# Kernel tuning notes

Measured on AMD Instinct MI355X. Metric: run time of the kernel, lower is better.

The kernel has to match this reference:

```python
import jax, jax.numpy as jnp
import numpy as np

D_MODEL = 768
EXPAND = 2
D_INNER = EXPAND * D_MODEL  # 1536
D_STATE = 16
D_CONV = 4
DT_RANK = D_MODEL // 16  # 48
N_LAYER = 3
BATCH, SEQLEN = 2, 1024
EPS = 1e-5


def setup_inputs() -> dict:
    key = jax.random.key(0)
    ks = jax.random.split(key, 8)
    s = 0.02
    hidden_states = jax.random.normal(ks[0], (BATCH, SEQLEN, D_MODEL), jnp.float32)
    norm_w = jnp.ones((N_LAYER, D_MODEL), jnp.float32)
    in_proj_w = s * jax.random.normal(ks[1], (N_LAYER, 2 * D_INNER, D_MODEL), jnp.float32)
    conv_w = s * jax.random.normal(ks[2], (N_LAYER, D_INNER, D_CONV), jnp.float32)
    conv_b = jnp.zeros((N_LAYER, D_INNER), jnp.float32)
    x_proj_w = s * jax.random.normal(ks[3], (N_LAYER, DT_RANK + 2 * D_STATE, D_INNER), jnp.float32)
    dt_proj_w = s * jax.random.normal(ks[4], (N_LAYER, D_INNER, DT_RANK), jnp.float32)
    dt_proj_b = jnp.full((N_LAYER, D_INNER), -4.6, jnp.float32)  # softplus ~ 0.01
    # S4D-real init: A_log = log(1..d_state), tiled over channels
    A_log = jnp.tile(jnp.log(jnp.arange(1, D_STATE + 1, dtype=jnp.float32))[None, None, :], (N_LAYER, D_INNER, 1))
    D_skip = jnp.ones((N_LAYER, D_INNER), jnp.float32)
    out_proj_w = s * jax.random.normal(ks[5], (N_LAYER, D_MODEL, D_INNER), jnp.float32)
    norm_f_w = jnp.ones((D_MODEL,), jnp.float32)
    return dict(hidden_states=hidden_states, norm_w=norm_w, in_proj_w=in_proj_w,
                conv_w=conv_w, conv_b=conv_b, x_proj_w=x_proj_w, dt_proj_w=dt_proj_w,
                dt_proj_b=dt_proj_b, A_log=A_log, D_skip=D_skip, out_proj_w=out_proj_w,
                norm_f_w=norm_f_w)


def _rmsnorm(x, w):
    return x * jax.lax.rsqrt(jnp.mean(x * x, axis=-1, keepdims=True) + EPS) * w


def _causal_conv1d(x, w, b):
    # x: [B, L, D]; w: [D, K] depthwise; left-pad for causality
    xt = jnp.transpose(x, (0, 2, 1))  # [B, D, L]
    y = jax.lax.conv_general_dilated(xt, w[:, None, :], window_strides=(1,),
                                     padding=[(D_CONV - 1, 0)], feature_group_count=D_INNER)
    return jnp.transpose(y, (0, 2, 1)) + b


def _selective_scan(u, delta, A, Bc, Cc, Dp):
    # u, delta: [B, L, D]; A: [D, N]; Bc, Cc: [B, L, N]
    def step(h, inp):
        dt, bt, ct, ut = inp  # [B,D], [B,N], [B,N], [B,D]
        h = jnp.exp(dt[..., None] * A) * h + (dt * ut)[..., None] * bt[:, None, :]
        y = jnp.einsum('bdn,bn->bd', h, ct)
        return h, y
    h0 = jnp.zeros((u.shape[0], u.shape[2], A.shape[1]), u.dtype)
    xs = (jnp.swapaxes(delta, 0, 1), jnp.swapaxes(Bc, 0, 1), jnp.swapaxes(Cc, 0, 1), jnp.swapaxes(u, 0, 1))
    _, ys = jax.lax.scan(step, h0, xs)  # ys: [L, B, D]
    return jnp.swapaxes(ys, 0, 1) + u * Dp


def _mixer(h, in_w, cw, cb, xw, dtw, dtb, A_log, Dp, ow):
    xz = jnp.einsum('bld,ed->ble', h, in_w)  # [B, L, 2*D_INNER]
    x, z = xz[..., :D_INNER], xz[..., D_INNER:]
    x = jax.nn.silu(_causal_conv1d(x, cw, cb))
    x_dbl = jnp.einsum('bld,ed->ble', x, xw)
    dt = x_dbl[..., :DT_RANK]
    Bc = x_dbl[..., DT_RANK:DT_RANK + D_STATE]
    Cc = x_dbl[..., DT_RANK + D_STATE:]
    delta = jax.nn.softplus(jnp.einsum('blr,dr->bld', dt, dtw) + dtb)
    A = -jnp.exp(A_log)
    y = _selective_scan(x, delta, A, Bc, Cc, Dp)
    y = y * jax.nn.silu(z)
    return jnp.einsum('bld,ed->ble', y, ow)


def reference(hidden_states, norm_w, in_proj_w, conv_w, conv_b, x_proj_w, dt_proj_w,
              dt_proj_b, A_log, D_skip, out_proj_w, norm_f_w):
    hidden = hidden_states
    residual = None
    for i in range(N_LAYER):
        residual = hidden if residual is None else hidden + residual  # fused add
        hidden = _rmsnorm(residual, norm_w[i])
        hidden = _mixer(hidden, in_proj_w[i], conv_w[i], conv_b[i], x_proj_w[i],
                        dt_proj_w[i], dt_proj_b[i], A_log[i], D_skip[i], out_proj_w[i])
    # final fused add + RMSNorm (prenorm=False)
    return _rmsnorm(hidden + residual, norm_f_w)
```

## Files before the change

### kernel.cpp

```cpp
#include <hip/hip_runtime.h>
#include <math.h>

#define D_MODEL 768
#define D_INNER 1536
#define D_STATE 16
#define D_CONV 4
#define DT_RANK 48
#define N_LAYER 3
#define BATCH 2
#define SEQLEN 1024
#define NROWS (BATCH * SEQLEN)
#define XDBL_W (DT_RANK + 2 * D_STATE)
#define EPS 1e-5f

#define SCLEN 16
#define SDN 16
#define KSPLIT_X 8

typedef short bf16x8 __attribute__((ext_vector_type(8)));
typedef float f32x4 __attribute__((ext_vector_type(4)));

__device__ __forceinline__ ushort f2bf(float x) {
    union { float f; uint u; } v; v.f = x;
    uint r = v.u + 0x7fff + ((v.u >> 16) & 1);
    return (ushort)(r >> 16);
}

__device__ __forceinline__ void gload_lds16(const void* g, void* l) {
    __builtin_amdgcn_global_load_lds(
        (const __attribute__((address_space(1))) unsigned int*)g,
        (__attribute__((address_space(3))) unsigned int*)l, 16, 0, 0);
}

__global__ __launch_bounds__(256) void cvt_bf16_kernel(
    const float* __restrict__ s, ushort* __restrict__ d, int n4)
{
    int i = blockIdx.x * 256 + threadIdx.x;
    if (i >= n4) return;
    float4 v = ((const float4*)s)[i];
    ushort4 o;
    o.x = f2bf(v.x); o.y = f2bf(v.y); o.z = f2bf(v.z); o.w = f2bf(v.w);
    ((ushort4*)d)[i] = o;
}

__global__ __launch_bounds__(256) void cvt_xw_pad_kernel(
    const float* __restrict__ src, ushort* __restrict__ dst)
{
    const int per = 128 * 1536 / 4;
    int i = blockIdx.x * 256 + threadIdx.x;
    if (i >= 3 * per) return;
    int li = i / per, rem = i - li * per;
    int r = (rem * 4) / 1536, c = (rem * 4) % 1536;
    ushort4 o = make_ushort4(0, 0, 0, 0);
    if (r < XDBL_W) {
        const float* s = src + ((size_t)li * XDBL_W + r) * 1536 + c;
        o.x = f2bf(s[0]); o.y = f2bf(s[1]); o.z = f2bf(s[2]); o.w = f2bf(s[3]);
    }
    ((ushort4*)dst)[i] = o;
}

__global__ __launch_bounds__(256) void cvt_dtw_pad_kernel(
    const float* __restrict__ src, ushort* __restrict__ dst)
{
    const int per = 1536 * 64 / 4;
    int i = blockIdx.x * 256 + threadIdx.x;
    if (i >= 3 * per) return;
    int li = i / per, rem = i - li * per;
    int r = (rem * 4) / 64, c = (rem * 4) % 64;
    ushort4 o = make_ushort4(0, 0, 0, 0);
    if (c < DT_RANK) {
        const float* s = src + ((size_t)li * 1536 + r) * DT_RANK + c;
        o.x = f2bf(s[0]); o.y = f2bf(s[1]); o.z = f2bf(s[2]); o.w = f2bf(s[3]);
    }
    ((ushort4*)dst)[i] = o;
}

__global__ __launch_bounds__(256) void add_rmsnorm_kernel(
    const float* __restrict__ x, const float* __restrict__ res_in,
    const float* __restrict__ w, float* __restrict__ res_out,
    float* __restrict__ normed_f32, ushort* __restrict__ normed_bf)
{
    int row = blockIdx.x;
    int tid = threadIdx.x;
    const float* xr = x + row * D_MODEL;
    float v[3];
    float ss = 0.f;
#pragma unroll
    for (int i = 0; i < 3; i++) {
        int c = tid + i * 256;
        float t = xr[c];
        if (res_in) t += res_in[row * D_MODEL + c];
        v[i] = t;
        ss += t * t;
    }
    for (int off = 32; off; off >>= 1) ss += __shfl_xor(ss, off, 64);
    __shared__ float red[4];
    if ((tid & 63) == 0) red[tid >> 6] = ss;
    __syncthreads();
    float tot = red[0] + red[1] + red[2] + red[3];
    float scale = rsqrtf(tot * (1.f / D_MODEL) + EPS);
#pragma unroll
    for (int i = 0; i < 3; i++) {
        int c = tid + i * 256;
        if (res_out) res_out[row * D_MODEL + c] = v[i];
        float o = v[i] * scale * w[c];
        if (normed_f32) normed_f32[row * D_MODEL + c] = o;
        if (normed_bf)  normed_bf[row * D_MODEL + c] = f2bf(o);
    }
}

template <int BM, int BN, int EPI, int SPLITK>
__global__ __launch_bounds__(256) void gemm_mfma_kernel(
    const ushort* __restrict__ A, const ushort* __restrict__ W,
    const float* __restrict__ bias, float* __restrict__ C,
    int ldc, int Nout, int M, int K)
{
    constexpr int TM = BM / 32;
    constexpr int TN = BN / 32;
    __shared__ __attribute__((aligned(16))) ushort As[BM * 64];
    __shared__ __attribute__((aligned(16))) ushort Ws[BN * 64];
    const int t = threadIdx.x;
    const int lane = t & 63, w = t >> 6;
    const int ln15 = lane & 15, q = lane >> 4;
    const int row0 = blockIdx.y * BM, col0 = blockIdx.x * BN;
    const int wm0 = (w & 1) * (BM / 2), wn0 = (w >> 1) * (BN / 2);

    int kper = K / SPLITK;
    int kz = (SPLITK > 1) ? blockIdx.z * kper : 0;
    if (SPLITK > 1) C += (size_t)blockIdx.z * M * ldc;

    f32x4 acc[TM][TN];
#pragma unroll
    for (int i = 0; i < TM; i++)
#pragma unroll
        for (int j = 0; j < TN; j++) acc[i][j] = (f32x4){0.f, 0.f, 0.f, 0.f};

    for (int k0 = kz; k0 < kz + kper; k0 += 64) {
        __syncthreads();
#pragma unroll
        for (int i = 0; i < BM / 32; i++) {
            int p = (i * 4 + w) * 64 + lane;
            int r = p >> 3, s = p & 7;
            int g = s ^ (r & 7);
            gload_lds16(A + (size_t)(row0 + r) * K + k0 + g * 8, &As[p * 8]);
        }
#pragma unroll
        for (int i = 0; i < BN / 32; i++) {
            int p = (i * 4 + w) * 64 + lane;
            int r = p >> 3, s = p & 7;
            int g = s ^ (r & 7);
            gload_lds16(W + (size_t)(col0 + r) * K + k0 + g * 8, &Ws[p * 8]);
        }
        __syncthreads();
#pragma unroll
        for (int ks = 0; ks < 2; ks++) {
            bf16x8 af[TM], wf[TN];
#pragma unroll
            for (int im = 0; im < TM; im++) {
                int m = wm0 + im * 16 + ln15;
                int slot = (ks * 4 + q) ^ (m & 7);
                af[im] = *(const bf16x8*)&As[m * 64 + slot * 8];
            }
#pragma unroll
            for (int jn = 0; jn < TN; jn++) {
                int n = wn0 + jn * 16 + ln15;
                int slot = (ks * 4 + q) ^ (n & 7);
                wf[jn] = *(const bf16x8*)&Ws[n * 64 + slot * 8];
            }
#pragma unroll
            for (int im = 0; im < TM; im++)
#pragma unroll
                for (int jn = 0; jn < TN; jn++)
                    acc[im][jn] = __builtin_amdgcn_mfma_f32_16x16x32_bf16(
                        af[im], wf[jn], acc[im][jn], 0, 0, 0);
        }
    }
#pragma unroll
    for (int im = 0; im < TM; im++) {
#pragma unroll
        for (int jn = 0; jn < TN; jn++) {
            int rr = row0 + wm0 + im * 16 + q * 4;
            int cc = col0 + wn0 + jn * 16 + ln15;
            if (cc < Nout) {
                float* cp = C + (size_t)rr * ldc + cc;
#pragma unroll
                for (int r = 0; r < 4; r++) {
                    float v = acc[im][jn][r];
                    if (EPI == 1) {
                        v += bias[cc];
                        v = (v > 20.f) ? v : log1pf(__expf(v));
                    }
                    cp[(size_t)r * ldc] = v;
                }
            }
        }
    }
}

__global__ __launch_bounds__(256) void xreduce_kernel(
    const float* __restrict__ Cp, float* __restrict__ xdbl,
    ushort* __restrict__ xdt)
{
    const int S4 = NROWS * XDBL_W / 4;
    int i = blockIdx.x * 256 + threadIdx.x;
    if (i >= S4) return;
    const float4* p = (const float4*)Cp;
    float4 o = p[i];
#pragma unroll
    for (int z = 1; z < KSPLIT_X; z++) {
        float4 a = p[i + (size_t)z * S4];
        o.x += a.x; o.y += a.y; o.z += a.z; o.w += a.w;
    }
    ((float4*)xdbl)[i] = o;
    int row = (i * 4) / XDBL_W, c0 = (i * 4) % XDBL_W;
    if (c0 < DT_RANK) {
        ushort4 b;
        b.x = f2bf(o.x); b.y = f2bf(o.y); b.z = f2bf(o.z); b.w = f2bf(o.w);
        *(ushort4*)&xdt[(size_t)row * 64 + c0] = b;
    } else if (c0 < 64) {
        *(ushort4*)&xdt[(size_t)row * 64 + c0] = make_ushort4(0, 0, 0, 0);
    }
}

__global__ __launch_bounds__(256) void conv_silu_kernel(
    const float* __restrict__ xz, const float* __restrict__ cw,
    const float* __restrict__ cb, float* __restrict__ out,
    ushort* __restrict__ out_bf)
{
    int idx = blockIdx.x * 256 + threadIdx.x;
    int d = idx % D_INNER;
    int bl = idx / D_INNER;
    int l = bl % SEQLEN;
    float s = cb[d];
    const float* xp = xz + (size_t)bl * (2 * D_INNER) + d;
#pragma unroll
    for (int k = 0; k < D_CONV; k++) {
        int ls = l - (D_CONV - 1) + k;
        if (ls >= 0) s += cw[d * D_CONV + k] * xp[(k - (D_CONV - 1)) * (2 * D_INNER)];
    }
    float sil = s / (1.f + __expf(-s));
    out[(size_t)bl * D_INNER + d] = sil;
    out_bf[(size_t)bl * D_INNER + d] = f2bf(sil);
}

__global__ __launch_bounds__(1024) void scan2_kernel(
    const float* __restrict__ u, const float* __restrict__ delta,
    const float* __restrict__ A_log, const float* __restrict__ xdbl,
    const float* __restrict__ Dskip, const float* __restrict__ xz,
    ushort* __restrict__ ybf)
{
    __shared__ float PL[16][SDN * 17];
    __shared__ float HL[16][SDN * 17];
    const int t = threadIdx.x;
    const int lane = t & 63;
    const int w = t >> 6;
    const int dsub = lane & 15;
    const int csub = lane >> 4;
    const int c = w * 4 + csub;
    const int b = blockIdx.x / (D_INNER / SDN);
    const int d = (blockIdx.x % (D_INNER / SDN)) * SDN + dsub;

    float a2[D_STATE];
#pragma unroll
    for (int n = 0; n < D_STATE; n++)
        a2[n] = -__expf(A_log[d * D_STATE + n]) * 1.44269504f;

    const size_t base = (size_t)b * SEQLEN * D_INNER + d;
    const float* dtp = delta + base;
    const float* up  = u + base;
    const float* xrow = xdbl + (size_t)b * SEQLEN * XDBL_W;
    const int l0 = c * SCLEN;

    float h[D_STATE], P[D_STATE];
#pragma unroll
    for (int n = 0; n < D_STATE; n++) { h[n] = 0.f; P[n] = 1.f; }

    for (int i = 0; i < SCLEN; i++) {
        const int l = l0 + i;
        float dt = dtp[(size_t)l * D_INNER];
        float uu = up[(size_t)l * D_INNER];
        const float4* Bv = (const float4*)(xrow + (size_t)l * XDBL_W + DT_RANK);
        float4 q0 = Bv[0], q1 = Bv[1], q2 = Bv[2], q3 = Bv[3];
        float Bf[D_STATE] = {q0.x,q0.y,q0.z,q0.w, q1.x,q1.y,q1.z,q1.w,
                             q2.x,q2.y,q2.z,q2.w, q3.x,q3.y,q3.z,q3.w};
        float dtu = dt * uu;
#pragma unroll
        for (int n = 0; n < D_STATE; n++) {
            float e = __builtin_amdgcn_exp2f(dt * a2[n]);
            P[n] *= e;
            h[n] = e * h[n] + dtu * Bf[n];
        }
    }

#pragma unroll
    for (int n = 0; n < D_STATE; n++) {
        float Pp = __shfl(P[n], lane - 16, 64);
        float Hp = __shfl(h[n], lane - 16, 64);
        bool act = csub >= 1;
        h[n] = act ? P[n] * Hp + h[n] : h[n];
        P[n] = act ? P[n] * Pp : P[n];
    }
#pragma unroll
    for (int n = 0; n < D_STATE; n++) {
        float Pp = __shfl(P[n], lane - 32, 64);
        float Hp = __shfl(h[n], lane - 32, 64);
        bool act = csub >= 2;
        h[n] = act ? P[n] * Hp + h[n] : h[n];
        P[n] = act ? P[n] * Pp : P[n];
    }

    if (csub == 3) {
#pragma unroll
        for (int n = 0; n < D_STATE; n++) {
            PL[w][dsub * 17 + n] = P[n];
            HL[w][dsub * 17 + n] = h[n];
        }
    }
    __syncthreads();

    if (t < SDN * D_STATE) {
        const int d2 = t >> 4, n2 = t & 15;
        float hin = 0.f;
        for (int ww = 0; ww < 16; ww++) {
            float Pw = PL[ww][d2 * 17 + n2];
            float Hw = HL[ww][d2 * 17 + n2];
            HL[ww][d2 * 17 + n2] = hin;
            hin = Pw * hin + Hw;
        }
    }
    __syncthreads();

#pragma unroll
    for (int n = 0; n < D_STATE; n++) {
        float Win = HL[w][dsub * 17 + n];
        float Pe = __shfl(P[n], lane - 16, 64);
        float He = __shfl(h[n], lane - 16, 64);
        h[n] = (csub == 0) ? Win : Pe * Win + He;
    }

    const float Dsk = Dskip[d];
    const float* zp = xz + (size_t)b * SEQLEN * (2 * D_INNER) + D_INNER + d;
    ushort* yp = ybf + base;
    for (int i = 0; i < SCLEN; i++) {
        const int l = l0 + i;
        float dt = dtp[(size_t)l * D_INNER];
        float uu = up[(size_t)l * D_INNER];
        float zz = zp[(size_t)l * (2 * D_INNER)];
        const float4* Bv = (const float4*)(xrow + (size_t)l * XDBL_W + DT_RANK);
        float4 q0 = Bv[0], q1 = Bv[1], q2 = Bv[2], q3 = Bv[3];
        float4 r0 = Bv[4], r1 = Bv[5], r2 = Bv[6], r3 = Bv[7];
        float Bf[D_STATE] = {q0.x,q0.y,q0.z,q0.w, q1.x,q1.y,q1.z,q1.w,
                             q2.x,q2.y,q2.z,q2.w, q3.x,q3.y,q3.z,q3.w};
        float Cf[D_STATE] = {r0.x,r0.y,r0.z,r0.w, r1.x,r1.y,r1.z,r1.w,
                             r2.x,r2.y,r2.z,r2.w, r3.x,r3.y,r3.z,r3.w};
        float dtu = dt * uu;
        float acc = 0.f;
#pragma unroll
        for (int n = 0; n < D_STATE; n++) {
            float e = __builtin_amdgcn_exp2f(dt * a2[n]);
            h[n] = e * h[n] + dtu * Bf[n];
            acc += h[n] * Cf[n];
        }
        float yy = acc + uu * Dsk;
        float ee = __builtin_amdgcn_exp2f(-zz * 1.44269504f);
        float sil = zz * __builtin_amdgcn_rcpf(1.f + ee);
        yp[(size_t)l * D_INNER] = f2bf(yy * sil);
    }
}

extern "C" void kernel_launch(void* const* d_in, const int* in_sizes, int n_in,
                              void* d_out, int out_size, void* d_ws, size_t ws_size,
                              hipStream_t stream)
{
    const float* hs        = (const float*)d_in[0];
    const float* norm_w    = (const float*)d_in[1];
    const float* in_proj_w = (const float*)d_in[2];
    const float* conv_w    = (const float*)d_in[3];
    const float* conv_b    = (const float*)d_in[4];
    const float* x_proj_w  = (const float*)d_in[5];
    const float* dt_proj_w = (const float*)d_in[6];
    const float* dt_proj_b = (const float*)d_in[7];
    const float* A_log     = (const float*)d_in[8];
    const float* D_skip    = (const float*)d_in[9];
    const float* out_proj_w= (const float*)d_in[10];
    const float* norm_f_w  = (const float*)d_in[11];

    float* ws = (float*)d_ws;
    float* residual = ws;
    float* hidden   = residual + NROWS * D_MODEL;
    float* xz       = hidden + NROWS * D_MODEL;
    float* xconv    = xz + NROWS * 2 * D_INNER;
    float* xdbl     = xconv + NROWS * D_INNER;
    float* delta    = xdbl + NROWS * XDBL_W;
    float* xpart    = delta + NROWS * D_INNER;
    ushort* normbf  = (ushort*)(xpart + (size_t)KSPLIT_X * NROWS * XDBL_W);
    ushort* ybf     = normbf + NROWS * D_MODEL;
    ushort* xconvbf = ybf + NROWS * D_INNER;
    ushort* xdtbf   = xconvbf + NROWS * D_INNER;
    ushort* win_bf  = xdtbf + NROWS * 64;
    ushort* wout_bf = win_bf + (size_t)N_LAYER * 2 * D_INNER * D_MODEL;
    ushort* xw_pad  = wout_bf + (size_t)N_LAYER * D_MODEL * D_INNER;
    ushort* dtw_pad = xw_pad + (size_t)N_LAYER * 128 * 1536;

    {
        int n_in4  = N_LAYER * 2 * D_INNER * D_MODEL / 4;
        int n_out4 = N_LAYER * D_MODEL * D_INNER / 4;
        cvt_bf16_kernel<<<(n_in4 + 255) / 256, 256, 0, stream>>>(in_proj_w, win_bf, n_in4);
        cvt_bf16_kernel<<<(n_out4 + 255) / 256, 256, 0, stream>>>(out_proj_w, wout_bf, n_out4);
        cvt_xw_pad_kernel<<<(3 * 128 * 1536 / 4 + 255) / 256, 256, 0, stream>>>(x_proj_w, xw_pad);
        cvt_dtw_pad_kernel<<<(3 * 1536 * 64 / 4 + 255) / 256, 256, 0, stream>>>(dt_proj_w, dtw_pad);
    }

    for (int i = 0; i < N_LAYER; i++) {
        add_rmsnorm_kernel<<<NROWS, 256, 0, stream>>>(
            i == 0 ? hs : hidden, i == 0 ? nullptr : residual,
            norm_w + i * D_MODEL, residual, nullptr, normbf);
        gemm_mfma_kernel<64, 128, 0, 1><<<dim3(2 * D_INNER / 128, NROWS / 64), 256, 0, stream>>>(
            normbf, win_bf + (size_t)i * 2 * D_INNER * D_MODEL, nullptr,
            xz, 2 * D_INNER, 2 * D_INNER, NROWS, D_MODEL);
        conv_silu_kernel<<<NROWS * D_INNER / 256, 256, 0, stream>>>(
            xz, conv_w + i * D_INNER * D_CONV, conv_b + i * D_INNER, xconv, xconvbf);
        gemm_mfma_kernel<64, 128, 0, KSPLIT_X><<<dim3(1, NROWS / 64, KSPLIT_X), 256, 0, stream>>>(
            xconvbf, xw_pad + (size_t)i * 128 * 1536, nullptr,
            xpart, XDBL_W, XDBL_W, NROWS, D_INNER);
        xreduce_kernel<<<(NROWS * XDBL_W / 4 + 255) / 256, 256, 0, stream>>>(
            xpart, xdbl, xdtbf);
        gemm_mfma_kernel<128, 128, 1, 1><<<dim3(D_INNER / 128, NROWS / 128), 256, 0, stream>>>(
            xdtbf, dtw_pad + (size_t)i * 1536 * 64, dt_proj_b + i * D_INNER,
            delta, D_INNER, D_INNER, NROWS, 64);
        scan2_kernel<<<BATCH * (D_INNER / SDN), 1024, 0, stream>>>(
            xconv, delta, A_log + (size_t)i * D_INNER * D_STATE, xdbl,
            D_skip + i * D_INNER, xz, ybf);
        gemm_mfma_kernel<64, 64, 0, 1><<<dim3(D_MODEL / 64, NROWS / 64), 256, 0, stream>>>(
            ybf, wout_bf + (size_t)i * D_MODEL * D_INNER, nullptr,
            hidden, D_MODEL, D_MODEL, NROWS, D_INNER);
    }
    add_rmsnorm_kernel<<<NROWS, 256, 0, stream>>>(
        hidden, residual, norm_f_w, nullptr, (float*)d_out, nullptr);
}
```

Before: 497.9 us.

## Store xz and conv output in bf16, drop split-K x_proj, merge weight converts

The in_proj GEMM now writes xz directly as bf16, and the conv kernel emits only bf16, so the scan reads u and z as bf16. The split-K x_proj GEMM and its reduction kernel are replaced by a single 32-row-tile GEMM whose epilogue writes the fp32 xdbl and the padded bf16 dt input. The four weight-conversion kernels merge into one launch, and the dt_proj tile size changes. These steps cut intermediate memory traffic and launch count, at the cost of bf16 rounding on u and z inside the scan and less parallelism in the x_proj GEMM.

```diff
diff --git a/kernel.cpp b/kernel.cpp
--- a/kernel.cpp
+++ b/kernel.cpp
@@ -15,7 +15,6 @@
 
 #define SCLEN 16
 #define SDN 16
-#define KSPLIT_X 8
 
 typedef short bf16x8 __attribute__((ext_vector_type(8)));
 typedef float f32x4 __attribute__((ext_vector_type(4)));
@@ -25,6 +24,10 @@
     uint r = v.u + 0x7fff + ((v.u >> 16) & 1);
     return (ushort)(r >> 16);
 }
+__device__ __forceinline__ float bf2f(ushort x) {
+    union { uint u; float f; } v; v.u = ((uint)x) << 16;
+    return v.f;
+}
 
 __device__ __forceinline__ void gload_lds16(const void* g, void* l) {
     __builtin_amdgcn_global_load_lds(
@@ -32,47 +35,54 @@
         (__attribute__((address_space(3))) unsigned int*)l, 16, 0, 0);
 }
 
-__global__ __launch_bounds__(256) void cvt_bf16_kernel(
-    const float* __restrict__ s, ushort* __restrict__ d, int n4)
+#define CVT_N0 (3 * 3072 * 768 / 4)
+#define CVT_N1 (3 * 768 * 1536 / 4)
+#define CVT_N2 (3 * 128 * 1536 / 4)
+#define CVT_N3 (3 * 1536 * 64 / 4)
+#define CVT_C1 (CVT_N0)
+#define CVT_C2 (CVT_C1 + CVT_N1)
+#define CVT_C3 (CVT_C2 + CVT_N2)
+#define CVT_TOT (CVT_C3 + CVT_N3)
+
+__global__ __launch_bounds__(256) void cvt_all_kernel(
+    const float* __restrict__ w_in, const float* __restrict__ w_out,
+    const float* __restrict__ w_x, const float* __restrict__ w_dt,
+    ushort* __restrict__ d_in, ushort* __restrict__ d_out,
+    ushort* __restrict__ d_x, ushort* __restrict__ d_dt)
 {
     int i = blockIdx.x * 256 + threadIdx.x;
-    if (i >= n4) return;
-    float4 v = ((const float4*)s)[i];
-    ushort4 o;
-    o.x = f2bf(v.x); o.y = f2bf(v.y); o.z = f2bf(v.z); o.w = f2bf(v.w);
-    ((ushort4*)d)[i] = o;
-}
-
-__global__ __launch_bounds__(256) void cvt_xw_pad_kernel(
-    const float* __restrict__ src, ushort* __restrict__ dst)
-{
-    const int per = 128 * 1536 / 4;
-    int i = blockIdx.x * 256 + threadIdx.x;
-    if (i >= 3 * per) return;
-    int li = i / per, rem = i - li * per;
-    int r = (rem * 4) / 1536, c = (rem * 4) % 1536;
-    ushort4 o = make_ushort4(0, 0, 0, 0);
-    if (r < XDBL_W) {
-        const float* s = src + ((size_t)li * XDBL_W + r) * 1536 + c;
-        o.x = f2bf(s[0]); o.y = f2bf(s[1]); o.z = f2bf(s[2]); o.w = f2bf(s[3]);
-    }
-    ((ushort4*)dst)[i] = o;
-}
-
-__global__ __launch_bounds__(256) void cvt_dtw_pad_kernel(
-    const float* __restrict__ src, ushort* __restrict__ dst)
-{
-    const int per = 1536 * 64 / 4;
-    int i = blockIdx.x * 256 + threadIdx.x;
-    if (i >= 3 * per) return;
-    int li = i / per, rem = i - li * per;
-    int r = (rem * 4) / 64, c = (rem * 4) % 64;
-    ushort4 o = make_ushort4(0, 0, 0, 0);
-    if (c < DT_RANK) {
-        const float* s = src + ((size_t)li * 1536 + r) * DT_RANK + c;
-        o.x = f2bf(s[0]); o.y = f2bf(s[1]); o.z = f2bf(s[2]); o.w = f2bf(s[3]);
-    }
-    ((ushort4*)dst)[i] = o;
+    if (i < CVT_C1) {
+        float4 v = ((const float4*)w_in)[i];
+        ushort4 o; o.x = f2bf(v.x); o.y = f2bf(v.y); o.z = f2bf(v.z); o.w = f2bf(v.w);
+        ((ushort4*)d_in)[i] = o;
+    } else if (i < CVT_C2) {
+        int j = i - CVT_C1;
+        float4 v = ((const float4*)w_out)[j];
+        ushort4 o; o.x = f2bf(v.x); o.y = f2bf(v.y); o.z = f2bf(v.z); o.w = f2bf(v.w);
+        ((ushort4*)d_out)[j] = o;
+    } else if (i < CVT_C3) {
+        int j = i - CVT_C2;
+        const int per = 128 * 1536 / 4;
+        int li = j / per, rem = j - li * per;
+        int r = (rem * 4) / 1536, c = (rem * 4) % 1536;
+        ushort4 o = make_ushort4(0, 0, 0, 0);
+        if (r < XDBL_W) {
+            const float* s = w_x + ((size_t)li * XDBL_W + r) * 1536 + c;
+            o.x = f2bf(s[0]); o.y = f2bf(s[1]); o.z = f2bf(s[2]); o.w = f2bf(s[3]);
+        }
+        ((ushort4*)d_x)[j] = o;
+    } else if (i < CVT_TOT) {
+        int j = i - CVT_C3;
+        const int per = 1536 * 64 / 4;
+        int li = j / per, rem = j - li * per;
+        int r = (rem * 4) / 64, c = (rem * 4) % 64;
+        ushort4 o = make_ushort4(0, 0, 0, 0);
+        if (c < DT_RANK) {
+            const float* s = w_dt + ((size_t)li * 1536 + r) * DT_RANK + c;
+            o.x = f2bf(s[0]); o.y = f2bf(s[1]); o.z = f2bf(s[2]); o.w = f2bf(s[3]);
+        }
+        ((ushort4*)d_dt)[j] = o;
+    }
 }
 
 __global__ __launch_bounds__(256) void add_rmsnorm_kernel(
@@ -109,11 +119,11 @@
     }
 }
 
-template <int BM, int BN, int EPI, int SPLITK>
+template <int BM, int BN, int EPI, int OUTBF>
 __global__ __launch_bounds__(256) void gemm_mfma_kernel(
     const ushort* __restrict__ A, const ushort* __restrict__ W,
-    const float* __restrict__ bias, float* __restrict__ C,
-    int ldc, int Nout, int M, int K)
+    const float* __restrict__ bias, void* __restrict__ Cv,
+    ushort* __restrict__ C2, int ldc, int Nout, int M, int K)
 {
     constexpr int TM = BM / 32;
     constexpr int TN = BN / 32;
@@ -125,9 +135,8 @@
     const int row0 = blockIdx.y * BM, col0 = blockIdx.x * BN;
     const int wm0 = (w & 1) * (BM / 2), wn0 = (w >> 1) * (BN / 2);
 
-    int kper = K / SPLITK;
-    int kz = (SPLITK > 1) ? blockIdx.z * kper : 0;
-    if (SPLITK > 1) C += (size_t)blockIdx.z * M * ldc;
+    float* Cf = (float*)Cv;
+    ushort* Cb = (ushort*)Cv;
 
     f32x4 acc[TM][TN];
 #pragma unroll
@@ -135,7 +144,7 @@
 #pragma unroll
         for (int j = 0; j < TN; j++) acc[i][j] = (f32x4){0.f, 0.f, 0.f, 0.f};
 
-    for (int k0 = kz; k0 < kz + kper; k0 += 64) {
+    for (int k0 = 0; k0 < K; k0 += 64) {
         __syncthreads();
 #pragma unroll
         for (int i = 0; i < BM / 32; i++) {
@@ -181,72 +190,49 @@
         for (int jn = 0; jn < TN; jn++) {
             int rr = row0 + wm0 + im * 16 + q * 4;
             int cc = col0 + wn0 + jn * 16 + ln15;
-            if (cc < Nout) {
-                float* cp = C + (size_t)rr * ldc + cc;
-#pragma unroll
-                for (int r = 0; r < 4; r++) {
-                    float v = acc[im][jn][r];
+#pragma unroll
+            for (int r = 0; r < 4; r++) {
+                float v = acc[im][jn][r];
+                if (EPI == 2) {
+                    if (cc < Nout) Cf[(size_t)(rr + r) * ldc + cc] = v;
+                    if (cc < DT_RANK)  C2[(size_t)(rr + r) * 64 + cc] = f2bf(v);
+                    else if (cc < 64)  C2[(size_t)(rr + r) * 64 + cc] = 0;
+                } else if (cc < Nout) {
                     if (EPI == 1) {
                         v += bias[cc];
                         v = (v > 20.f) ? v : log1pf(__expf(v));
                     }
-                    cp[(size_t)r * ldc] = v;
+                    if (OUTBF) Cb[(size_t)(rr + r) * ldc + cc] = f2bf(v);
+                    else       Cf[(size_t)(rr + r) * ldc + cc] = v;
                 }
             }
         }
     }
 }
 
-__global__ __launch_bounds__(256) void xreduce_kernel(
-    const float* __restrict__ Cp, float* __restrict__ xdbl,
-    ushort* __restrict__ xdt)
-{
-    const int S4 = NROWS * XDBL_W / 4;
-    int i = blockIdx.x * 256 + threadIdx.x;
-    if (i >= S4) return;
-    const float4* p = (const float4*)Cp;
-    float4 o = p[i];
-#pragma unroll
-    for (int z = 1; z < KSPLIT_X; z++) {
-        float4 a = p[i + (size_t)z * S4];
-        o.x += a.x; o.y += a.y; o.z += a.z; o.w += a.w;
-    }
-    ((float4*)xdbl)[i] = o;
-    int row = (i * 4) / XDBL_W, c0 = (i * 4) % XDBL_W;
-    if (c0 < DT_RANK) {
-        ushort4 b;
-        b.x = f2bf(o.x); b.y = f2bf(o.y); b.z = f2bf(o.z); b.w = f2bf(o.w);
-        *(ushort4*)&xdt[(size_t)row * 64 + c0] = b;
-    } else if (c0 < 64) {
-        *(ushort4*)&xdt[(size_t)row * 64 + c0] = make_ushort4(0, 0, 0, 0);
-    }
-}
-
 __global__ __launch_bounds__(256) void conv_silu_kernel(
-    const float* __restrict__ xz, const float* __restrict__ cw,
-    const float* __restrict__ cb, float* __restrict__ out,
-    ushort* __restrict__ out_bf)
+    const ushort* __restrict__ xzbf, const float* __restrict__ cw,
+    const float* __restrict__ cb, ushort* __restrict__ out_bf)
 {
     int idx = blockIdx.x * 256 + threadIdx.x;
     int d = idx % D_INNER;
     int bl = idx / D_INNER;
     int l = bl % SEQLEN;
     float s = cb[d];
-    const float* xp = xz + (size_t)bl * (2 * D_INNER) + d;
+    const ushort* xp = xzbf + (size_t)bl * (2 * D_INNER) + d;
 #pragma unroll
     for (int k = 0; k < D_CONV; k++) {
         int ls = l - (D_CONV - 1) + k;
-        if (ls >= 0) s += cw[d * D_CONV + k] * xp[(k - (D_CONV - 1)) * (2 * D_INNER)];
+        if (ls >= 0) s += cw[d * D_CONV + k] * bf2f(xp[(k - (D_CONV - 1)) * (2 * D_INNER)]);
     }
     float sil = s / (1.f + __expf(-s));
-    out[(size_t)bl * D_INNER + d] = sil;
     out_bf[(size_t)bl * D_INNER + d] = f2bf(sil);
 }
 
 __global__ __launch_bounds__(1024) void scan2_kernel(
-    const float* __restrict__ u, const float* __restrict__ delta,
+    const ushort* __restrict__ ubf, const float* __restrict__ delta,
     const float* __restrict__ A_log, const float* __restrict__ xdbl,
-    const float* __restrict__ Dskip, const float* __restrict__ xz,
+    const float* __restrict__ Dskip, const ushort* __restrict__ xzbf,
     ushort* __restrict__ ybf)
 {
     __shared__ float PL[16][SDN * 17];
@@ -267,7 +253,7 @@
 
     const size_t base = (size_t)b * SEQLEN * D_INNER + d;
     const float* dtp = delta + base;
-    const float* up  = u + base;
+    const ushort* up = ubf + base;
     const float* xrow = xdbl + (size_t)b * SEQLEN * XDBL_W;
     const int l0 = c * SCLEN;
 
@@ -278,7 +264,7 @@
     for (int i = 0; i < SCLEN; i++) {
         const int l = l0 + i;
         float dt = dtp[(size_t)l * D_INNER];
-        float uu = up[(size_t)l * D_INNER];
+        float uu = bf2f(up[(size_t)l * D_INNER]);
         const float4* Bv = (const float4*)(xrow + (size_t)l * XDBL_W + DT_RANK);
         float4 q0 = Bv[0], q1 = Bv[1], q2 = Bv[2], q3 = Bv[3];
         float Bf[D_STATE] = {q0.x,q0.y,q0.z,q0.w, q1.x,q1.y,q1.z,q1.w,
@@ -339,13 +325,13 @@
     }
 
     const float Dsk = Dskip[d];
-    const float* zp = xz + (size_t)b * SEQLEN * (2 * D_INNER) + D_INNER + d;
+    const ushort* zp = xzbf + (size_t)b * SEQLEN * (2 * D_INNER) + D_INNER + d;
     ushort* yp = ybf + base;
     for (int i = 0; i < SCLEN; i++) {
         const int l = l0 + i;
         float dt = dtp[(size_t)l * D_INNER];
-        float uu = up[(size_t)l * D_INNER];
-        float zz = zp[(size_t)l * (2 * D_INNER)];
+        float uu = bf2f(up[(size_t)l * D_INNER]);
+        float zz = bf2f(zp[(size_t)l * (2 * D_INNER)]);
         const float4* Bv = (const float4*)(xrow + (size_t)l * XDBL_W + DT_RANK);
         float4 q0 = Bv[0], q1 = Bv[1], q2 = Bv[2], q3 = Bv[3];
         float4 r0 = Bv[4], r1 = Bv[5], r2 = Bv[6], r3 = Bv[7];
@@ -388,12 +374,10 @@
     float* ws = (float*)d_ws;
     float* residual = ws;
     float* hidden   = residual + NROWS * D_MODEL;
-    float* xz       = hidden + NROWS * D_MODEL;
-    float* xconv    = xz + NROWS * 2 * D_INNER;
-    float* xdbl     = xconv + NROWS * D_INNER;
+    float* xdbl     = hidden + NROWS * D_MODEL;
     float* delta    = xdbl + NROWS * XDBL_W;
-    float* xpart    = delta + NROWS * D_INNER;
-    ushort* normbf  = (ushort*)(xpart + (size_t)KSPLIT_X * NROWS * XDBL_W);
+    ushort* xzbf    = (ushort*)(delta + NROWS * D_INNER);
+    ushort* normbf  = xzbf + (size_t)NROWS * 2 * D_INNER;
     ushort* ybf     = normbf + NROWS * D_MODEL;
     ushort* xconvbf = ybf + NROWS * D_INNER;
     ushort* xdtbf   = xconvbf + NROWS * D_INNER;
@@ -402,14 +386,9 @@
     ushort* xw_pad  = wout_bf + (size_t)N_LAYER * D_MODEL * D_INNER;
     ushort* dtw_pad = xw_pad + (size_t)N_LAYER * 128 * 1536;
 
-    {
-        int n_in4  = N_LAYER * 2 * D_INNER * D_MODEL / 4;
-        int n_out4 = N_LAYER * D_MODEL * D_INNER / 4;
-        cvt_bf16_kernel<<<(n_in4 + 255) / 256, 256, 0, stream>>>(in_proj_w, win_bf, n_in4);
-        cvt_bf16_kernel<<<(n_out4 + 255) / 256, 256, 0, stream>>>(out_proj_w, wout_bf, n_out4);
-        cvt_xw_pad_kernel<<<(3 * 128 * 1536 / 4 + 255) / 256, 256, 0, stream>>>(x_proj_w, xw_pad);
-        cvt_dtw_pad_kernel<<<(3 * 1536 * 64 / 4 + 255) / 256, 256, 0, stream>>>(dt_proj_w, dtw_pad);
-    }
+    cvt_all_kernel<<<(CVT_TOT + 255) / 256, 256, 0, stream>>>(
+        in_proj_w, out_proj_w, x_proj_w, dt_proj_w,
+        win_bf, wout_bf, xw_pad, dtw_pad);
 
     for (int i = 0; i < N_LAYER; i++) {
         add_rmsnorm_kernel<<<NROWS, 256, 0, stream>>>(
@@ -417,23 +396,21 @@
             norm_w + i * D_MODEL, residual, nullptr, normbf);
         gemm_mfma_kernel<64, 128, 0, 1><<<dim3(2 * D_INNER / 128, NROWS / 64), 256, 0, stream>>>(
             normbf, win_bf + (size_t)i * 2 * D_INNER * D_MODEL, nullptr,
-            xz, 2 * D_INNER, 2 * D_INNER, NROWS, D_MODEL);
+            xzbf, nullptr, 2 * D_INNER, 2 * D_INNER, NROWS, D_MODEL);
         conv_silu_kernel<<<NROWS * D_INNER / 256, 256, 0, stream>>>(
-            xz, conv_w + i * D_INNER * D_CONV, conv_b + i * D_INNER, xconv, xconvbf);
-        gemm_mfma_kernel<64, 128, 0, KSPLIT_X><<<dim3(1, NROWS / 64, KSPLIT_X), 256, 0, stream>>>(
+            xzbf, conv_w + i * D_INNER * D_CONV, conv_b + i * D_INNER, xconvbf);
+        gemm_mfma_kernel<32, 128, 2, 0><<<dim3(1, NROWS / 32), 256, 0, stream>>>(
             xconvbf, xw_pad + (size_t)i * 128 * 1536, nullptr,
-            xpart, XDBL_W, XDBL_W, NROWS, D_INNER);
-        xreduce_kernel<<<(NROWS * XDBL_W / 4 + 255) / 256, 256, 0, stream>>>(
-            xpart, xdbl, xdtbf);
-        gemm_mfma_kernel<128, 128, 1, 1><<<dim3(D_INNER / 128, NROWS / 128), 256, 0, stream>>>(
+            xdbl, xdtbf, XDBL_W, XDBL_W, NROWS, D_INNER);
+        gemm_mfma_kernel<64, 128, 1, 0><<<dim3(D_INNER / 128, NROWS / 64), 256, 0, stream>>>(
             xdtbf, dtw_pad + (size_t)i * 1536 * 64, dt_proj_b + i * D_INNER,
-            delta, D_INNER, D_INNER, NROWS, 64);
+            delta, nullptr, D_INNER, D_INNER, NROWS, 64);
         scan2_kernel<<<BATCH * (D_INNER / SDN), 1024, 0, stream>>>(
-            xconv, delta, A_log + (size_t)i * D_INNER * D_STATE, xdbl,
-            D_skip + i * D_INNER, xz, ybf);
-        gemm_mfma_kernel<64, 64, 0, 1><<<dim3(D_MODEL / 64, NROWS / 64), 256, 0, stream>>>(
+            xconvbf, delta, A_log + (size_t)i * D_INNER * D_STATE, xdbl,
+            D_skip + i * D_INNER, xzbf, ybf);
+        gemm_mfma_kernel<64, 64, 0, 0><<<dim3(D_MODEL / 64, NROWS / 64), 256, 0, stream>>>(
             ybf, wout_bf + (size_t)i * D_MODEL * D_INNER, nullptr,
-            hidden, D_MODEL, D_MODEL, NROWS, D_INNER);
+            hidden, nullptr, D_MODEL, D_MODEL, NROWS, D_INNER);
     }
     add_rmsnorm_kernel<<<NROWS, 256, 0, stream>>>(
         hidden, residual, norm_f_w, nullptr, (float*)d_out, nullptr);
```

Result: no change. 501.9 us (+0.8%).
